# Performance work log

Measured on AMD Instinct MI355X. Metric: run time of the kernel, lower is better.

Reference implementation:

```python
import jax, jax.numpy as jnp
import numpy as np

N, E, H, C = 50000, 800000, 4, 32   # nodes, edges, heads, per-head channels
EMB = 64                              # embedding_dim
VOCAB = 1000                          # input_dim (label vocab)


def _gat_layer(x, src, dst, W, a_src, a_dst, b):
    """PyG GATConv (concat heads, negative_slope=0.2, self-loops already in src/dst)."""
    n = x.shape[0]
    h = (x @ W).reshape(n, H, -1)                 # [N,H,C]
    al_s = (h * a_src).sum(-1)                    # [N,H]
    al_d = (h * a_dst).sum(-1)                    # [N,H]
    e = jax.nn.leaky_relu(al_s[src] + al_d[dst], 0.2)   # [E',H]
    m = jax.ops.segment_max(e, dst, num_segments=n)     # segment softmax (stable)
    p = jnp.exp(e - m[dst])
    s = jax.ops.segment_sum(p, dst, num_segments=n)
    alpha = p / (s[dst] + 1e-16)                  # [E',H]
    out = jax.ops.segment_sum(h[src] * alpha[..., None], dst, num_segments=n)
    return out.reshape(n, -1) + b                 # [N,H*C]


def setup_inputs() -> dict:
    key = jax.random.key(0)
    ks = jax.random.split(key, 16)
    def w(k, shape):
        return jax.random.normal(k, shape, jnp.float32) * 0.1
    return dict(
        label=jax.random.randint(ks[0], (N,), 0, VOCAB),
        edge_index=jax.random.randint(ks[1], (2, E), 0, N),
        weight=jax.random.uniform(ks[2], (E,), jnp.float32),
        request_quantity=jax.random.uniform(ks[3], (N,), jnp.float32),
        emb_table=w(ks[4], (VOCAB, EMB)),
        req_W=w(ks[5], (1, EMB)),
        req_b=jnp.zeros((EMB,), jnp.float32),
        W0=w(ks[6], (2 * EMB, H * C)), a_src0=w(ks[7], (H, C)), a_dst0=w(ks[8], (H, C)), b0=jnp.zeros((H * C,), jnp.float32),
        W1=w(ks[9], (H * C, H * C)), a_src1=w(ks[10], (H, C)), a_dst1=w(ks[11], (H, C)), b1=jnp.zeros((H * C,), jnp.float32),
        W2=w(ks[12], (H * C, H * C)), a_src2=w(ks[13], (H, C)), a_dst2=w(ks[14], (H, C)), b2=jnp.zeros((H * C,), jnp.float32),
    )


def reference(label, edge_index, weight, request_quantity, emb_table, req_W, req_b,
              W0, a_src0, a_dst0, b0, W1, a_src1, a_dst1, b1, W2, a_src2, a_dst2, b2):
    del weight  # GATConv(edge_dim=None): edge weights are not used in attention
    x_emb = emb_table[label]                                  # [N,EMB]
    rq = request_quantity
    rq = (rq - rq.mean()) / (rq.std(ddof=1) + 1e-6)           # torch std uses ddof=1
    req = rq[:, None] @ req_W + req_b                         # [N,EMB]
    x = jnp.concatenate([x_emb, req], axis=-1)                # [N,2*EMB]
    # PyG GATConv adds self-loops by default
    loops = jnp.arange(N)
    src = jnp.concatenate([edge_index[0], loops])
    dst = jnp.concatenate([edge_index[1], loops])
    gelu = lambda t: jax.nn.gelu(t, approximate=False)        # torch nn.GELU is exact
    x = gelu(_gat_layer(x, src, dst, W0, a_src0, a_dst0, b0))
    x = gelu(_gat_layer(x, src, dst, W1, a_src1, a_dst1, b1))
    x = gelu(_gat_layer(x, src, dst, W2, a_src2, a_dst2, b2))
    return x
```

## Files before the change

kernel.cpp:

```cpp
#include <hip/hip_runtime.h>
#include <hip/hip_fp16.h>
#include <math.h>

#define NN 50000
#define NE 800000
#define HC 128
#define EMB 64
#define STATS_BLOCKS 64
#define NB 196
#define HIST_BLOCKS 196
#define WPREP_BLOCKS 192
#define WT_ROW 136
#define GEMM_BLOCKS 782

typedef _Float16 f16x8 __attribute__((ext_vector_type(8)));
typedef float f32x4 __attribute__((ext_vector_type(4)));

__device__ __forceinline__ float lrelu(float x) { return x > 0.0f ? x : 0.2f * x; }
__device__ __forceinline__ float gelu_f(float x) {
    return 0.5f * x * (1.0f + erff(x * 0.70710678118654752440f));
}
__device__ __forceinline__ float sel4(float4 v, int h) {
    float r = v.x;
    r = (h == 1) ? v.y : r;
    r = (h == 2) ? v.z : r;
    r = (h == 3) ? v.w : r;
    return r;
}
__device__ __forceinline__ f16x8 cvt8(float4 a, float4 b) {
    f16x8 v;
    v[0] = (_Float16)a.x; v[1] = (_Float16)a.y; v[2] = (_Float16)a.z; v[3] = (_Float16)a.w;
    v[4] = (_Float16)b.x; v[5] = (_Float16)b.y; v[6] = (_Float16)b.z; v[7] = (_Float16)b.w;
    return v;
}

__global__ void prep_kernel(const float* __restrict__ rq, float* __restrict__ stats,
                            const int* __restrict__ dst, int* __restrict__ bucketCnt,
                            const float* __restrict__ W0, const float* __restrict__ W1,
                            const float* __restrict__ W2, _Float16* __restrict__ wt) {
    __shared__ float ls[4], ls2[4];
    __shared__ int cnt[NB];
    if (blockIdx.x < STATS_BLOCKS) {
        int i = blockIdx.x * 256 + threadIdx.x;
        float s = 0.f, s2 = 0.f;
        for (; i < NN; i += STATS_BLOCKS * 256) {
            float v = rq[i];
            s += v; s2 += v * v;
        }
        #pragma unroll
        for (int off = 32; off > 0; off >>= 1) {
            s  += __shfl_down(s, off);
            s2 += __shfl_down(s2, off);
        }
        int lane = threadIdx.x & 63, wid = threadIdx.x >> 6;
        if (lane == 0) { ls[wid] = s; ls2[wid] = s2; }
        __syncthreads();
        if (threadIdx.x == 0) {
            atomicAdd(&stats[0], ls[0] + ls[1] + ls[2] + ls[3]);
            atomicAdd(&stats[1], ls2[0] + ls2[1] + ls2[2] + ls2[3]);
        }
    } else if (blockIdx.x < STATS_BLOCKS + HIST_BLOCKS) {
        int bb = blockIdx.x - STATS_BLOCKS;
        for (int i = threadIdx.x; i < NB; i += 256) cnt[i] = 0;
        __syncthreads();
        int base = bb * 4096;
        #pragma unroll
        for (int it = 0; it < 16; it++) {
            int i = base + it * 256 + threadIdx.x;
            if (i < NE) atomicAdd(&cnt[dst[i] >> 8], 1);
        }
        __syncthreads();
        for (int i = threadIdx.x; i < NB; i += 256)
            if (cnt[i]) atomicAdd(&bucketCnt[i], cnt[i]);
    } else {
        int bb = blockIdx.x - STATS_BLOCKS - HIST_BLOCKS;
        int l = bb >> 6, blk = bb & 63;
        const float* W = (l == 0) ? W0 : (l == 1) ? W1 : W2;
        int idx = blk * 256 + threadIdx.x;
        int n = idx >> 7, k = idx & 127;
        wt[(size_t)l * 128 * WT_ROW + n * WT_ROW + k] = (_Float16)W[k * 128 + n];
    }
}

__device__ __forceinline__ void scan_buckets(const int* __restrict__ bucketCnt,
                                             int* sIncl ) {
    int t = threadIdx.x;
    int v = (t < NB) ? bucketCnt[t] : 0;
    sIncl[t] = v;
    __syncthreads();
    #pragma unroll
    for (int off = 1; off < 256; off <<= 1) {
        int add = (t >= off) ? sIncl[t - off] : 0;
        __syncthreads();
        sIncl[t] += add;
        __syncthreads();
    }
}

__device__ __forceinline__ void mfma_epilogue(_Float16* sWt, _Float16* sX,
        const float* __restrict__ a_src, const float* __restrict__ a_dst,
        __half* __restrict__ h, float* __restrict__ als, float* __restrict__ ald,
        int row0) {
    int t = threadIdx.x;
    int w = t >> 6, l = t & 63;
    int col = l & 15, quad = l >> 4;

    f16x8 afr[4];
    #pragma unroll
    for (int ks = 0; ks < 4; ks++)
        afr[ks] = *(const f16x8*)&sX[(w * 16 + col) * WT_ROW + ks * 32 + quad * 8];

    f32x4 zero = {0.f, 0.f, 0.f, 0.f};
    f32x4 acc[8];
    #pragma unroll
    for (int nt = 0; nt < 8; nt++) acc[nt] = zero;
    #pragma unroll
    for (int nt = 0; nt < 8; nt++) {
        #pragma unroll
        for (int ks = 0; ks < 4; ks++) {
            f16x8 bfr = *(const f16x8*)&sWt[(nt * 16 + col) * WT_ROW + ks * 32 + quad * 8];
            acc[nt] = __builtin_amdgcn_mfma_f32_16x16x32_f16(afr[ks], bfr, acc[nt], 0, 0, 0);
        }
    }
    __syncthreads();

    _Float16* sOut = sWt;
    #pragma unroll
    for (int nt = 0; nt < 8; nt++)
        #pragma unroll
        for (int r = 0; r < 4; r++)
            sOut[(w * 16 + quad * 4 + r) * WT_ROW + nt * 16 + col] = (_Float16)acc[nt][r];
    __builtin_amdgcn_wave_barrier();
    #pragma unroll
    for (int i = 0; i < 4; i++) {
        int u = l + 64 * i;
        int r = u >> 4, off = (u & 15) * 8;
        int rr = row0 + w * 16 + r;
        f16x8 v = *(const f16x8*)&sOut[(w * 16 + r) * WT_ROW + off];
        if (rr < NN) *(f16x8*)(h + (size_t)rr * 128 + off) = v;
    }

    float as[8], ad[8];
    #pragma unroll
    for (int nt = 0; nt < 8; nt++) {
        as[nt] = a_src[nt * 16 + col];
        ad[nt] = a_dst[nt * 16 + col];
    }
    #pragma unroll
    for (int r = 0; r < 4; r++) {
        float ps[4], pd[4];
        #pragma unroll
        for (int hd = 0; hd < 4; hd++) {
            ps[hd] = acc[2 * hd][r] * as[2 * hd] + acc[2 * hd + 1][r] * as[2 * hd + 1];
            pd[hd] = acc[2 * hd][r] * ad[2 * hd] + acc[2 * hd + 1][r] * ad[2 * hd + 1];
            ps[hd] += __shfl_xor(ps[hd], 1); pd[hd] += __shfl_xor(pd[hd], 1);
            ps[hd] += __shfl_xor(ps[hd], 2); pd[hd] += __shfl_xor(pd[hd], 2);
            ps[hd] += __shfl_xor(ps[hd], 4); pd[hd] += __shfl_xor(pd[hd], 4);
            ps[hd] += __shfl_xor(ps[hd], 8); pd[hd] += __shfl_xor(pd[hd], 8);
        }
        int rr = row0 + w * 16 + quad * 4 + r;
        if (col == 0 && rr < NN) {
            *(float4*)(als + (size_t)rr * 4) = make_float4(ps[0], ps[1], ps[2], ps[3]);
            *(float4*)(ald + (size_t)rr * 4) = make_float4(pd[0], pd[1], pd[2], pd[3]);
        }
    }
}

__launch_bounds__(256)
__global__ void gemm0_binA_kernel(const _Float16* __restrict__ wt,
                                  const float* __restrict__ a_src, const float* __restrict__ a_dst,
                                  __half* __restrict__ h, float* __restrict__ als,
                                  float* __restrict__ ald,
                                  const int* __restrict__ label, const float* __restrict__ rq,
                                  const float* __restrict__ emb, const float* __restrict__ reqW,
                                  const float* __restrict__ reqb, const float* __restrict__ stats,
                                  const int* __restrict__ src, const int* __restrict__ dst,
                                  const int* __restrict__ bucketCnt, int* __restrict__ gcur,
                                  int2* __restrict__ edge_tmp) {
    extern __shared__ char smem[];
    if (blockIdx.x >= GEMM_BLOCKS) {
        int bb = blockIdx.x - GEMM_BLOCKS;
        int* sIncl  = (int*)smem;
        int* sBaseE = sIncl + 256;
        int* cnt    = sBaseE + 256;
        int* cur    = cnt + NB;
        int t = threadIdx.x;
        scan_buckets(bucketCnt, sIncl);
        {
            int v = (t < NB) ? bucketCnt[t] : 0;
            sBaseE[t] = sIncl[t] - v;
        }
        for (int i = t; i < NB; i += 256) cnt[i] = 0;
        __syncthreads();
        int base = bb * 4096;
        int d[16], s[16];
        #pragma unroll
        for (int it = 0; it < 16; it++) {
            int i = base + it * 256 + t;
            bool ok = i < NE;
            d[it] = ok ? dst[i] : -1;
            s[it] = ok ? src[i] : 0;
            if (ok) atomicAdd(&cnt[d[it] >> 8], 1);
        }
        __syncthreads();
        for (int i = t; i < NB; i += 256)
            cur[i] = cnt[i] ? (sBaseE[i] + atomicAdd(&gcur[i], cnt[i])) : 0;
        __syncthreads();
        #pragma unroll
        for (int it = 0; it < 16; it++) {
            if (d[it] >= 0) {
                int b = d[it] >> 8;
                int pos = atomicAdd(&cur[b], 1);
                edge_tmp[pos] = make_int2(s[it], d[it] & 255);
            }
        }
        return;
    }
    _Float16* sWt = (_Float16*)smem;
    _Float16* sX  = sWt + 128 * WT_ROW;
    int t = threadIdx.x;
    int row0 = blockIdx.x * 64;

    {
        const f16x8* g = (const f16x8*)wt;
        f16x8* s = (f16x8*)sWt;
        #pragma unroll
        for (int i = 0; i < 9; i++) {
            int idx = t + 256 * i;
            if (idx < 128 * WT_ROW / 8) s[idx] = g[idx];
        }
    }
    {
        float sum = stats[0], sumsq = stats[1];
        float mean = sum / (float)NN;
        float var = (sumsq - sum * sum / (float)NN) / (float)(NN - 1);
        float inv = 1.0f / (sqrtf(var) + 1e-6f);
        #pragma unroll
        for (int i = 0; i < 4; i++) {
            int idx = t + 256 * i;
            int r = idx >> 4;
            int q = idx & 15;
            int rr = row0 + r;
            f16x8 v;
            #pragma unroll
            for (int j = 0; j < 8; j++) v[j] = (_Float16)0.f;
            if (rr < NN) {
                if (q < 8) {
                    const float4* er = (const float4*)(emb + (size_t)label[rr] * EMB);
                    v = cvt8(er[q * 2], er[q * 2 + 1]);
                } else {
                    int j4 = (q - 8) * 2;
                    float4 w0 = ((const float4*)reqW)[j4],     b0 = ((const float4*)reqb)[j4];
                    float4 w1 = ((const float4*)reqW)[j4 + 1], b1 = ((const float4*)reqb)[j4 + 1];
                    float r2 = (rq[rr] - mean) * inv;
                    v = cvt8(make_float4(r2 * w0.x + b0.x, r2 * w0.y + b0.y,
                                         r2 * w0.z + b0.z, r2 * w0.w + b0.w),
                             make_float4(r2 * w1.x + b1.x, r2 * w1.y + b1.y,
                                         r2 * w1.z + b1.z, r2 * w1.w + b1.w));
                }
            }
            *(f16x8*)&sX[r * WT_ROW + q * 8] = v;
        }
    }
    __syncthreads();
    mfma_epilogue(sWt, sX, a_src, a_dst, h, als, ald, row0);
}

__global__ void binB_kernel(const int2* __restrict__ edge_tmp, const int* __restrict__ bucketCnt,
                            int* __restrict__ row_start, int* __restrict__ src_sorted) {
    __shared__ int sIncl[256];
    __shared__ int ldeg[256];
    __shared__ int lexcl[256];
    __shared__ int lcur[256];
    __shared__ int s_base, s_end;
    int b = blockIdx.x, t = threadIdx.x;
    scan_buckets(bucketCnt, sIncl);
    if (t == 0) {
        s_end = sIncl[b];
        s_base = sIncl[b] - bucketCnt[b];
    }
    ldeg[t] = 0;
    __syncthreads();
    int base = s_base, endb = s_end;
    for (int i = base + t; i < endb; i += 256)
        atomicAdd(&ldeg[edge_tmp[i].y], 1);
    __syncthreads();
    int v = ldeg[t];
    lexcl[t] = v;
    __syncthreads();
    #pragma unroll
    for (int off = 1; off < 256; off <<= 1) {
        int add = (t >= off) ? lexcl[t - off] : 0;
        __syncthreads();
        lexcl[t] += add;
        __syncthreads();
    }
    int excl = lexcl[t] - v;
    int node = b * 256 + t;
    if (node <= NN) row_start[node] = base + excl;
    lcur[t] = excl;
    __syncthreads();
    for (int i = base + t; i < endb; i += 256) {
        int2 e = edge_tmp[i];
        int pos = atomicAdd(&lcur[e.y], 1);
        src_sorted[base + pos] = e.x;
    }
}

__launch_bounds__(256)
__global__ void layer_fused_kernel(const __half* __restrict__ hp, const float* __restrict__ alsp,
                                   const float* __restrict__ aldp, const int* __restrict__ row_start,
                                   const int* __restrict__ src_sorted, const float* __restrict__ biasp,
                                   const _Float16* __restrict__ wt,
                                   const float* __restrict__ a_src, const float* __restrict__ a_dst,
                                   __half* __restrict__ ho, float* __restrict__ also_,
                                   float* __restrict__ aldo) {
    __shared__ _Float16 sX[64 * WT_ROW];
    __shared__ int2 lds_sp[4][4][130];
    int t = threadIdx.x;
    int w = t >> 6, lane = t & 63;
    int g    = lane >> 4;
    int cg   = lane & 15;
    int c0   = cg * 8;
    int head = cg >> 2;
    int row0 = blockIdx.x * 64;

    for (int round = 0; round < 4; round++) {
        int nb = row0 + w * 16 + round * 4;
        if (nb >= NN) continue;
        int node = nb + g;

        int rs = row_start[node];
        int re = row_start[node + 1];
        int start = __shfl(rs, 0);
        int end   = __shfl(re, 48);
        int b1 = __shfl(rs, 16), b2 = __shfl(rs, 32), b3 = __shfl(rs, 48);

        float4 adv = *(const float4*)(aldp + (size_t)node * 4);
        float4 avs = *(const float4*)(alsp + (size_t)node * 4);

        float p_self = __expf(lrelu(sel4(avs, head) + sel4(adv, head)));
        float s_sum = p_self;
        float acc[8];
        {
            f16x8 hv = *(const f16x8*)(hp + (size_t)node * 128 + c0);
            #pragma unroll
            for (int j = 0; j < 8; j++) acc[j] = (float)hv[j] * p_self;
        }

        for (int base = start; base < end; base += 128) {
            int j0 = base + lane, j1 = base + 64 + lane;
            bool v0 = j0 < end, v1 = j1 < end;
            int my0 = v0 ? src_sorted[j0] : 0;
            int my1 = v1 ? src_sorted[j1] : 0;
            float4 av0 = *(const float4*)(alsp + (size_t)my0 * 4);
            float4 av1 = *(const float4*)(alsp + (size_t)my1 * 4);
            int o0 = (j0 >= b1) + (j0 >= b2) + (j0 >= b3);
            int o1 = (j1 >= b1) + (j1 >= b2) + (j1 >= b3);
            float4 d0 = *(const float4*)(aldp + (size_t)(nb + (o0 > 3 ? 3 : o0)) * 4);
            float4 d1 = *(const float4*)(aldp + (size_t)(nb + (o1 > 3 ? 3 : o1)) * 4);
            lds_sp[w][0][lane] = make_int2(my0, __float_as_int(__expf(lrelu(av0.x + d0.x))));
            lds_sp[w][1][lane] = make_int2(my0, __float_as_int(__expf(lrelu(av0.y + d0.y))));
            lds_sp[w][2][lane] = make_int2(my0, __float_as_int(__expf(lrelu(av0.z + d0.z))));
            lds_sp[w][3][lane] = make_int2(my0, __float_as_int(__expf(lrelu(av0.w + d0.w))));
            lds_sp[w][0][64 + lane] = make_int2(my1, __float_as_int(__expf(lrelu(av1.x + d1.x))));
            lds_sp[w][1][64 + lane] = make_int2(my1, __float_as_int(__expf(lrelu(av1.y + d1.y))));
            lds_sp[w][2][64 + lane] = make_int2(my1, __float_as_int(__expf(lrelu(av1.z + d1.z))));
            lds_sp[w][3][64 + lane] = make_int2(my1, __float_as_int(__expf(lrelu(av1.w + d1.w))));
            __builtin_amdgcn_wave_barrier();

            int lo  = rs > base ? rs : base;
            int hiw = base + 128;
            int hi  = re < hiw ? re : hiw;
            for (int k = lo; k < hi; k += 8) {
                float p[8];
                const __half* ap[8];
                #pragma unroll
                for (int i = 0; i < 8; i++) {
                    int e = k + i;
                    bool val = e < hi;
                    int ec = (val ? e : hi - 1) - base;
                    int2 sp = lds_sp[w][head][ec];
                    p[i] = val ? __int_as_float(sp.y) : 0.f;
                    ap[i] = hp + (size_t)sp.x * 128 + c0;
                }
                f16x8 raw[8];
                #pragma unroll
                for (int i = 0; i < 8; i++)
                    raw[i] = *(const f16x8*)ap[i];
                #pragma unroll
                for (int i = 0; i < 8; i++) {
                    s_sum += p[i];
                    #pragma unroll
                    for (int jj = 0; jj < 8; jj++)
                        acc[jj] += (float)raw[i][jj] * p[i];
                }
            }
            __builtin_amdgcn_wave_barrier();
        }

        float invs = 1.0f / (s_sum + 1e-16f);
        float4 bv0 = *(const float4*)(biasp + c0);
        float4 bv1 = *(const float4*)(biasp + c0 + 4);
        float ob[8] = {bv0.x, bv0.y, bv0.z, bv0.w, bv1.x, bv1.y, bv1.z, bv1.w};
        f16x8 o;
        #pragma unroll
        for (int jj = 0; jj < 8; jj++)
            o[jj] = (_Float16)gelu_f(acc[jj] * invs + ob[jj]);
        *(f16x8*)&sX[(w * 16 + round * 4 + g) * WT_ROW + c0] = o;
    }
    __builtin_amdgcn_wave_barrier();

    int col = cg, quad = g;
    f16x8 afr[4];
    #pragma unroll
    for (int ks = 0; ks < 4; ks++)
        afr[ks] = *(const f16x8*)&sX[(w * 16 + col) * WT_ROW + ks * 32 + quad * 8];
    __builtin_amdgcn_wave_barrier();

    f32x4 zero = {0.f, 0.f, 0.f, 0.f};
    f32x4 acc2[8];
    #pragma unroll
    for (int nt = 0; nt < 8; nt++) acc2[nt] = zero;
    #pragma unroll
    for (int nt = 0; nt < 8; nt++) {
        #pragma unroll
        for (int ks = 0; ks < 4; ks++) {
            f16x8 bfr = *(const f16x8*)&wt[(nt * 16 + col) * WT_ROW + ks * 32 + quad * 8];
            acc2[nt] = __builtin_amdgcn_mfma_f32_16x16x32_f16(afr[ks], bfr, acc2[nt], 0, 0, 0);
        }
    }

    _Float16* sOut = sX;
    #pragma unroll
    for (int nt = 0; nt < 8; nt++)
        #pragma unroll
        for (int r = 0; r < 4; r++)
            sOut[(w * 16 + quad * 4 + r) * WT_ROW + nt * 16 + col] = (_Float16)acc2[nt][r];
    __builtin_amdgcn_wave_barrier();
    #pragma unroll
    for (int i = 0; i < 4; i++) {
        int u = lane + 64 * i;
        int r = u >> 4, off2 = (u & 15) * 8;
        int rr = row0 + w * 16 + r;
        f16x8 v = *(const f16x8*)&sOut[(w * 16 + r) * WT_ROW + off2];
        if (rr < NN) *(f16x8*)(ho + (size_t)rr * 128 + off2) = v;
    }

    float as[8], ad[8];
    #pragma unroll
    for (int nt = 0; nt < 8; nt++) {
        as[nt] = a_src[nt * 16 + col];
        ad[nt] = a_dst[nt * 16 + col];
    }
    #pragma unroll
    for (int r = 0; r < 4; r++) {
        float ps[4], pd[4];
        #pragma unroll
        for (int hd = 0; hd < 4; hd++) {
            ps[hd] = acc2[2 * hd][r] * as[2 * hd] + acc2[2 * hd + 1][r] * as[2 * hd + 1];
            pd[hd] = acc2[2 * hd][r] * ad[2 * hd] + acc2[2 * hd + 1][r] * ad[2 * hd + 1];
            ps[hd] += __shfl_xor(ps[hd], 1); pd[hd] += __shfl_xor(pd[hd], 1);
            ps[hd] += __shfl_xor(ps[hd], 2); pd[hd] += __shfl_xor(pd[hd], 2);
            ps[hd] += __shfl_xor(ps[hd], 4); pd[hd] += __shfl_xor(pd[hd], 4);
            ps[hd] += __shfl_xor(ps[hd], 8); pd[hd] += __shfl_xor(pd[hd], 8);
        }
        int rr = row0 + w * 16 + quad * 4 + r;
        if (col == 0 && rr < NN) {
            *(float4*)(also_ + (size_t)rr * 4) = make_float4(ps[0], ps[1], ps[2], ps[3]);
            *(float4*)(aldo + (size_t)rr * 4) = make_float4(pd[0], pd[1], pd[2], pd[3]);
        }
    }
}

__launch_bounds__(256)
__global__ void agg_final_kernel(const __half* __restrict__ h, const float* __restrict__ als_,
                                 const float* __restrict__ ald_, const int* __restrict__ row_start,
                                 const int* __restrict__ src_sorted, const float* __restrict__ bias,
                                 float* __restrict__ outf) {
    __shared__ int2 lds_sp[4][4][130];
    int wid  = threadIdx.x >> 6;
    int lane = threadIdx.x & 63;
    int g    = lane >> 4;
    int cg   = lane & 15;
    int c0   = cg * 8;
    int head = cg >> 2;

    int nb = blockIdx.x * 16 + wid * 4;
    if (nb >= NN) return;
    int node = nb + g;

    int rs = row_start[node];
    int re = row_start[node + 1];
    int start = __shfl(rs, 0);
    int end   = __shfl(re, 48);
    int b1 = __shfl(rs, 16), b2 = __shfl(rs, 32), b3 = __shfl(rs, 48);

    float4 adv = *(const float4*)(ald_ + (size_t)node * 4);
    float4 avs = *(const float4*)(als_ + (size_t)node * 4);

    float p_self = __expf(lrelu(sel4(avs, head) + sel4(adv, head)));
    float s_sum = p_self;
    float acc[8];
    {
        f16x8 hv = *(const f16x8*)(h + (size_t)node * 128 + c0);
        #pragma unroll
        for (int j = 0; j < 8; j++) acc[j] = (float)hv[j] * p_self;
    }

    for (int base = start; base < end; base += 128) {
        int j0 = base + lane, j1 = base + 64 + lane;
        bool v0 = j0 < end, v1 = j1 < end;
        int my0 = v0 ? src_sorted[j0] : 0;
        int my1 = v1 ? src_sorted[j1] : 0;
        float4 av0 = *(const float4*)(als_ + (size_t)my0 * 4);
        float4 av1 = *(const float4*)(als_ + (size_t)my1 * 4);
        int o0 = (j0 >= b1) + (j0 >= b2) + (j0 >= b3);
        int o1 = (j1 >= b1) + (j1 >= b2) + (j1 >= b3);
        float4 d0 = *(const float4*)(ald_ + (size_t)(nb + (o0 > 3 ? 3 : o0)) * 4);
        float4 d1 = *(const float4*)(ald_ + (size_t)(nb + (o1 > 3 ? 3 : o1)) * 4);
        lds_sp[wid][0][lane] = make_int2(my0, __float_as_int(__expf(lrelu(av0.x + d0.x))));
        lds_sp[wid][1][lane] = make_int2(my0, __float_as_int(__expf(lrelu(av0.y + d0.y))));
        lds_sp[wid][2][lane] = make_int2(my0, __float_as_int(__expf(lrelu(av0.z + d0.z))));
        lds_sp[wid][3][lane] = make_int2(my0, __float_as_int(__expf(lrelu(av0.w + d0.w))));
        lds_sp[wid][0][64 + lane] = make_int2(my1, __float_as_int(__expf(lrelu(av1.x + d1.x))));
        lds_sp[wid][1][64 + lane] = make_int2(my1, __float_as_int(__expf(lrelu(av1.y + d1.y))));
        lds_sp[wid][2][64 + lane] = make_int2(my1, __float_as_int(__expf(lrelu(av1.z + d1.z))));
        lds_sp[wid][3][64 + lane] = make_int2(my1, __float_as_int(__expf(lrelu(av1.w + d1.w))));
        __builtin_amdgcn_wave_barrier();

        int lo  = rs > base ? rs : base;
        int hiw = base + 128;
        int hi  = re < hiw ? re : hiw;
        for (int k = lo; k < hi; k += 16) {
            float p[16];
            const __half* ap[16];
            #pragma unroll
            for (int i = 0; i < 16; i++) {
                int e = k + i;
                bool val = e < hi;
                int ec = (val ? e : hi - 1) - base;
                int2 sp = lds_sp[wid][head][ec];
                p[i] = val ? __int_as_float(sp.y) : 0.f;
                ap[i] = h + (size_t)sp.x * 128 + c0;
            }
            f16x8 raw[16];
            #pragma unroll
            for (int i = 0; i < 16; i++)
                raw[i] = *(const f16x8*)ap[i];
            #pragma unroll
            for (int i = 0; i < 16; i++) {
                s_sum += p[i];
                #pragma unroll
                for (int jj = 0; jj < 8; jj++)
                    acc[jj] += (float)raw[i][jj] * p[i];
            }
        }
        __builtin_amdgcn_wave_barrier();
    }

    float invs = 1.0f / (s_sum + 1e-16f);
    float4 bv0 = *(const float4*)(bias + c0);
    float4 bv1 = *(const float4*)(bias + c0 + 4);
    float ob[8] = {bv0.x, bv0.y, bv0.z, bv0.w, bv1.x, bv1.y, bv1.z, bv1.w};
    float o8[8];
    #pragma unroll
    for (int jj = 0; jj < 8; jj++) o8[jj] = gelu_f(acc[jj] * invs + ob[jj]);
    float* op = outf + (size_t)node * 128 + c0;
    *(float4*)op       = make_float4(o8[0], o8[1], o8[2], o8[3]);
    *(float4*)(op + 4) = make_float4(o8[4], o8[5], o8[6], o8[7]);
}

extern "C" void kernel_launch(void* const* d_in, const int* in_sizes, int n_in,
                              void* d_out, int out_size, void* d_ws, size_t ws_size,
                              hipStream_t stream) {
    const int*   label = (const int*)d_in[0];
    const int*   eidx  = (const int*)d_in[1];
    const float* rq    = (const float*)d_in[3];
    const float* emb   = (const float*)d_in[4];
    const float* reqW  = (const float*)d_in[5];
    const float* reqb  = (const float*)d_in[6];
    const float* W[3]    = {(const float*)d_in[7],  (const float*)d_in[11], (const float*)d_in[15]};
    const float* asrc[3] = {(const float*)d_in[8],  (const float*)d_in[12], (const float*)d_in[16]};
    const float* adst[3] = {(const float*)d_in[9],  (const float*)d_in[13], (const float*)d_in[17]};
    const float* bias[3] = {(const float*)d_in[10], (const float*)d_in[14], (const float*)d_in[18]};

    const int* e_src = eidx;
    const int* e_dst = eidx + NE;

    char* ws = (char*)d_ws;
    size_t off = 0;
    auto A = [&](size_t n) { size_t o = off; off += (n + 255) & ~(size_t)255; return o; };
    size_t o_bcnt  = A(256 * 4);
    size_t o_gcur  = A(256 * 4);
    size_t o_stats = A(8);
    size_t zero_bytes = off;
    size_t o_row   = A((size_t)(NN + 1) * 4);
    size_t o_etmp  = A((size_t)NE * 8);
    size_t o_srcS  = A((size_t)NE * 4);
    size_t o_wt    = A((size_t)3 * 128 * WT_ROW * 2);
    size_t o_h0    = A((size_t)NN * 128 * 2);
    size_t o_h1    = A((size_t)NN * 128 * 2);
    size_t o_als0  = A((size_t)NN * 4 * 4);
    size_t o_ald0  = A((size_t)NN * 4 * 4);
    size_t o_als1  = A((size_t)NN * 4 * 4);
    size_t o_ald1  = A((size_t)NN * 4 * 4);
    (void)ws_size; (void)n_in; (void)in_sizes; (void)out_size;

    int*      bcnt  = (int*)(ws + o_bcnt);
    int*      gcur  = (int*)(ws + o_gcur);
    float*    stats = (float*)(ws + o_stats);
    int*      rowst = (int*)(ws + o_row);
    int2*     etmp  = (int2*)(ws + o_etmp);
    int*      srcS  = (int*)(ws + o_srcS);
    _Float16* wt    = (_Float16*)(ws + o_wt);
    __half*   h0    = (__half*)(ws + o_h0);
    __half*   h1    = (__half*)(ws + o_h1);
    float*    als0  = (float*)(ws + o_als0);
    float*    ald0  = (float*)(ws + o_ald0);
    float*    als1  = (float*)(ws + o_als1);
    float*    ald1  = (float*)(ws + o_ald1);

    (void)hipMemsetAsync(ws, 0, zero_bytes, stream);

    const int smem_l0 = (128 + 64) * WT_ROW * 2;

    prep_kernel<<<STATS_BLOCKS + HIST_BLOCKS + WPREP_BLOCKS, 256, 0, stream>>>(
        rq, stats, e_dst, bcnt, W[0], W[1], W[2], wt);
    gemm0_binA_kernel<<<GEMM_BLOCKS + HIST_BLOCKS, 256, smem_l0, stream>>>(
        wt, asrc[0], adst[0], h0, als0, ald0, label, rq, emb, reqW, reqb, stats,
        e_src, e_dst, bcnt, gcur, etmp);
    binB_kernel<<<NB, 256, 0, stream>>>(etmp, bcnt, rowst, srcS);
    layer_fused_kernel<<<GEMM_BLOCKS, 256, 0, stream>>>(
        h0, als0, ald0, rowst, srcS, bias[0],
        wt + (size_t)1 * 128 * WT_ROW, asrc[1], adst[1], h1, als1, ald1);
    layer_fused_kernel<<<GEMM_BLOCKS, 256, 0, stream>>>(
        h1, als1, ald1, rowst, srcS, bias[1],
        wt + (size_t)2 * 128 * WT_ROW, asrc[2], adst[2], h0, als0, ald0);
    agg_final_kernel<<<(NN + 15) / 16, 256, 0, stream>>>(
        h0, als0, ald0, rowst, srcS, bias[2], (float*)d_out);
}
```

Before: 291.0 us.

## Run fused GAT layer with one wave per block and 16-edge gather batches

The fused aggregate+GEMM layer kernel changes from 256-thread blocks covering 64 nodes to 64-thread blocks covering 16 nodes, which shrinks shared memory per block and gives the scheduler finer-grained blocks for load balancing across irregular degrees. The inner gather loop is unrolled from 8 to 16 edges, issuing more independent row loads per iteration to hide memory latency. In exchange, register pressure rises (launch bounds now request 3 waves per SIMD), which risks spills or lower occupancy. The NN>=node guard is dropped since 50000 is divisible by 16.

```diff
diff --git a/kernel.cpp b/kernel.cpp
--- a/kernel.cpp
+++ b/kernel.cpp
@@ -307,7 +307,7 @@
     }
 }
 
-__launch_bounds__(256)
+__launch_bounds__(64, 3)
 __global__ void layer_fused_kernel(const __half* __restrict__ hp, const float* __restrict__ alsp,
                                    const float* __restrict__ aldp, const int* __restrict__ row_start,
                                    const int* __restrict__ src_sorted, const float* __restrict__ biasp,
@@ -315,19 +315,17 @@
                                    const float* __restrict__ a_src, const float* __restrict__ a_dst,
                                    __half* __restrict__ ho, float* __restrict__ also_,
                                    float* __restrict__ aldo) {
-    __shared__ _Float16 sX[64 * WT_ROW];
-    __shared__ int2 lds_sp[4][4][130];
-    int t = threadIdx.x;
-    int w = t >> 6, lane = t & 63;
+    __shared__ _Float16 sX[16 * WT_ROW];
+    __shared__ int2 lds_sp[4][130];
+    int lane = threadIdx.x;
     int g    = lane >> 4;
     int cg   = lane & 15;
     int c0   = cg * 8;
     int head = cg >> 2;
-    int row0 = blockIdx.x * 64;
+    int row0 = blockIdx.x * 16;
 
     for (int round = 0; round < 4; round++) {
-        int nb = row0 + w * 16 + round * 4;
-        if (nb >= NN) continue;
+        int nb = row0 + round * 4;
         int node = nb + g;
 
         int rs = row_start[node];
@@ -359,37 +357,37 @@
             int o1 = (j1 >= b1) + (j1 >= b2) + (j1 >= b3);
             float4 d0 = *(const float4*)(aldp + (size_t)(nb + (o0 > 3 ? 3 : o0)) * 4);
             float4 d1 = *(const float4*)(aldp + (size_t)(nb + (o1 > 3 ? 3 : o1)) * 4);
-            lds_sp[w][0][lane] = make_int2(my0, __float_as_int(__expf(lrelu(av0.x + d0.x))));
-            lds_sp[w][1][lane] = make_int2(my0, __float_as_int(__expf(lrelu(av0.y + d0.y))));
-            lds_sp[w][2][lane] = make_int2(my0, __float_as_int(__expf(lrelu(av0.z + d0.z))));
-            lds_sp[w][3][lane] = make_int2(my0, __float_as_int(__expf(lrelu(av0.w + d0.w))));
-            lds_sp[w][0][64 + lane] = make_int2(my1, __float_as_int(__expf(lrelu(av1.x + d1.x))));
-            lds_sp[w][1][64 + lane] = make_int2(my1, __float_as_int(__expf(lrelu(av1.y + d1.y))));
-            lds_sp[w][2][64 + lane] = make_int2(my1, __float_as_int(__expf(lrelu(av1.z + d1.z))));
-            lds_sp[w][3][64 + lane] = make_int2(my1, __float_as_int(__expf(lrelu(av1.w + d1.w))));
+            lds_sp[0][lane] = make_int2(my0, __float_as_int(__expf(lrelu(av0.x + d0.x))));
+            lds_sp[1][lane] = make_int2(my0, __float_as_int(__expf(lrelu(av0.y + d0.y))));
+            lds_sp[2][lane] = make_int2(my0, __float_as_int(__expf(lrelu(av0.z + d0.z))));
+            lds_sp[3][lane] = make_int2(my0, __float_as_int(__expf(lrelu(av0.w + d0.w))));
+            lds_sp[0][64 + lane] = make_int2(my1, __float_as_int(__expf(lrelu(av1.x + d1.x))));
+            lds_sp[1][64 + lane] = make_int2(my1, __float_as_int(__expf(lrelu(av1.y + d1.y))));
+            lds_sp[2][64 + lane] = make_int2(my1, __float_as_int(__expf(lrelu(av1.z + d1.z))));
+            lds_sp[3][64 + lane] = make_int2(my1, __float_as_int(__expf(lrelu(av1.w + d1.w))));
             __builtin_amdgcn_wave_barrier();
 
             int lo  = rs > base ? rs : base;
             int hiw = base + 128;
             int hi  = re < hiw ? re : hiw;
-            for (int k = lo; k < hi; k += 8) {
-                float p[8];
-                const __half* ap[8];
+            for (int k = lo; k < hi; k += 16) {
+                float p[16];
+                const __half* ap[16];
                 #pragma unroll
-                for (int i = 0; i < 8; i++) {
+                for (int i = 0; i < 16; i++) {
                     int e = k + i;
                     bool val = e < hi;
                     int ec = (val ? e : hi - 1) - base;
-                    int2 sp = lds_sp[w][head][ec];
+                    int2 sp = lds_sp[head][ec];
                     p[i] = val ? __int_as_float(sp.y) : 0.f;
                     ap[i] = hp + (size_t)sp.x * 128 + c0;
                 }
-                f16x8 raw[8];
+                f16x8 raw[16];
                 #pragma unroll
-                for (int i = 0; i < 8; i++)
+                for (int i = 0; i < 16; i++)
                     raw[i] = *(const f16x8*)ap[i];
                 #pragma unroll
-                for (int i = 0; i < 8; i++) {
+                for (int i = 0; i < 16; i++) {
                     s_sum += p[i];
                     #pragma unroll
                     for (int jj = 0; jj < 8; jj++)
@@ -407,7 +405,7 @@
         #pragma unroll
         for (int jj = 0; jj < 8; jj++)
             o[jj] = (_Float16)gelu_f(acc[jj] * invs + ob[jj]);
-        *(f16x8*)&sX[(w * 16 + round * 4 + g) * WT_ROW + c0] = o;
+        *(f16x8*)&sX[(round * 4 + g) * WT_ROW + c0] = o;
     }
     __builtin_amdgcn_wave_barrier();
 
@@ -415,7 +413,7 @@
     f16x8 afr[4];
     #pragma unroll
     for (int ks = 0; ks < 4; ks++)
-        afr[ks] = *(const f16x8*)&sX[(w * 16 + col) * WT_ROW + ks * 32 + quad * 8];
+        afr[ks] = *(const f16x8*)&sX[col * WT_ROW + ks * 32 + quad * 8];
     __builtin_amdgcn_wave_barrier();
 
     f32x4 zero = {0.f, 0.f, 0.f, 0.f};
@@ -436,14 +434,14 @@
     for (int nt = 0; nt < 8; nt++)
         #pragma unroll
         for (int r = 0; r < 4; r++)
-            sOut[(w * 16 + quad * 4 + r) * WT_ROW + nt * 16 + col] = (_Float16)acc2[nt][r];
+            sOut[(quad * 4 + r) * WT_ROW + nt * 16 + col] = (_Float16)acc2[nt][r];
     __builtin_amdgcn_wave_barrier();
     #pragma unroll
     for (int i = 0; i < 4; i++) {
         int u = lane + 64 * i;
         int r = u >> 4, off2 = (u & 15) * 8;
-        int rr = row0 + w * 16 + r;
-        f16x8 v = *(const f16x8*)&sOut[(w * 16 + r) * WT_ROW + off2];
+        int rr = row0 + r;
+        f16x8 v = *(const f16x8*)&sOut[r * WT_ROW + off2];
         if (rr < NN) *(f16x8*)(ho + (size_t)rr * 128 + off2) = v;
     }
 
@@ -465,7 +463,7 @@
             ps[hd] += __shfl_xor(ps[hd], 4); pd[hd] += __shfl_xor(pd[hd], 4);
             ps[hd] += __shfl_xor(ps[hd], 8); pd[hd] += __shfl_xor(pd[hd], 8);
         }
-        int rr = row0 + w * 16 + quad * 4 + r;
+        int rr = row0 + quad * 4 + r;
         if (col == 0 && rr < NN) {
             *(float4*)(also_ + (size_t)rr * 4) = make_float4(ps[0], ps[1], ps[2], ps[3]);
             *(float4*)(aldo + (size_t)rr * 4) = make_float4(pd[0], pd[1], pd[2], pd[3]);
@@ -631,10 +629,10 @@
         wt, asrc[0], adst[0], h0, als0, ald0, label, rq, emb, reqW, reqb, stats,
         e_src, e_dst, bcnt, gcur, etmp);
     binB_kernel<<<NB, 256, 0, stream>>>(etmp, bcnt, rowst, srcS);
-    layer_fused_kernel<<<GEMM_BLOCKS, 256, 0, stream>>>(
+    layer_fused_kernel<<<(NN + 15) / 16, 64, 0, stream>>>(
         h0, als0, ald0, rowst, srcS, bias[0],
         wt + (size_t)1 * 128 * WT_ROW, asrc[1], adst[1], h1, als1, ald1);
-    layer_fused_kernel<<<GEMM_BLOCKS, 256, 0, stream>>>(
+    layer_fused_kernel<<<(NN + 15) / 16, 64, 0, stream>>>(
         h1, als1, ald1, rowst, srcS, bias[1],
         wt + (size_t)2 * 128 * WT_ROW, asrc[2], adst[2], h0, als0, ald0);
     agg_final_kernel<<<(NN + 15) / 16, 256, 0, stream>>>(
```

Measured after the change: 283.4 us (median of 2 runs). 2.6% less time.
